# Performance work log

Measured on AMD Instinct MI355X. Metric: run time of the kernel, lower is better.

Reference implementation:

```python
import jax, jax.numpy as jnp
import numpy as np

E, K = 8, 2            # num_experts, top_k
H, DFF = 1024, 2048    # embd_dim, d_ff
B, S = 4, 1024


def setup_inputs() -> dict:
    key = jax.random.key(0)
    ks = jax.random.split(key, 5)
    s_in = 1.0 / np.sqrt(H)
    s_ff = 1.0 / np.sqrt(DFF)
    return {
        "x": jax.random.normal(ks[0], (B, S, H), jnp.float32),
        "centroids": jax.random.normal(ks[1], (E, H), jnp.float32),
        # nn.Linear weights are [out, in]
        "gate_w": jax.random.normal(ks[2], (E, DFF, H), jnp.float32) * s_in,
        "up_w": jax.random.normal(ks[3], (E, DFF, H), jnp.float32) * s_in,
        "down_w": jax.random.normal(ks[4], (E, H, DFF), jnp.float32) * s_ff,
        "routing_bias": jnp.zeros((E,), jnp.float32),
    }


def reference(x, centroids, gate_w, up_w, down_w, routing_bias):
    Bb, Ss, Hh = x.shape
    xf = x.reshape(-1, Hh)  # [T, H]
    # sigmoid affinity router + (non-trainable) routing bias
    affinity = jax.nn.sigmoid(xf @ centroids.T)          # [T, E]
    topk_scores, topk_idx = jax.lax.top_k(affinity + routing_bias, K)  # [T, K]
    topk_w = jax.nn.softmax(topk_scores, axis=-1)        # [T, K]

    # Dense per-expert SwiGLU FFN on all tokens (same math as the
    # sort/gather grouped loop; selection happens in the gather below).
    g = jnp.einsum('th,efh->etf', xf, gate_w)            # [E, T, DFF]
    u = jnp.einsum('th,efh->etf', xf, up_w)              # [E, T, DFF]
    y = jnp.einsum('etf,ehf->eth', jax.nn.silu(g) * u, down_w)  # [E, T, H]

    yt = jnp.transpose(y, (1, 0, 2))                     # [T, E, H]
    sel = jnp.take_along_axis(yt, topk_idx[:, :, None], axis=1)  # [T, K, H]
    out_flat = jnp.sum(sel * topk_w[:, :, None], axis=1)  # [T, H]

    counts = jnp.bincount(topk_idx.ravel(), length=E)    # per-expert token counts
    return out_flat.reshape(Bb, Ss, Hh), counts
```

## Files before the change

kernel.cpp:

```cpp
#include <hip/hip_runtime.h>
#include <math.h>

constexpr int E = 8, H = 1024, DFF = 2048, T = 4096;
constexpr int TR = 8192;
constexpr int MAXJ = 72;

typedef __bf16 bf16x8 __attribute__((ext_vector_type(8)));
typedef __bf16 bf16x4 __attribute__((ext_vector_type(4)));
typedef float f32x4 __attribute__((ext_vector_type(4)));

__device__ __forceinline__ void gload16(const void* g, void* l) {
    __builtin_amdgcn_global_load_lds(
        (const __attribute__((address_space(1))) unsigned int*)g,
        (__attribute__((address_space(3))) unsigned int*)l, 16, 0, 0);
}

constexpr int CONV_BLOCKS = 3072;
__global__ __launch_bounds__(256) void k0_fused(
    const float* __restrict__ x, const float* __restrict__ cent,
    const float* __restrict__ bias,
    int* __restrict__ se, float* __restrict__ sw,
    const float* __restrict__ gw, __bf16* __restrict__ gwb,
    const float* __restrict__ uw, __bf16* __restrict__ uwb,
    __bf16* __restrict__ xb, float* __restrict__ outz,
    int w4, int x4, int o4, int* __restrict__ done) {
    __shared__ float cs[E * H];
    int tid = threadIdx.x;

    if (blockIdx.x == 0 && tid == 0) *done = 0;

    if (blockIdx.x >= 1024) {
        int total = 2 * w4 + x4 + o4;
        int stride = CONV_BLOCKS * 256;
        for (int i = (blockIdx.x - 1024) * 256 + tid; i < total; i += stride) {
            if (i >= 2 * w4 + x4) {
                float4 z = {0.f, 0.f, 0.f, 0.f};
                ((float4*)outz)[i - 2 * w4 - x4] = z;
                continue;
            }
            const float* in; __bf16* outp; int idx;
            if (i < w4) { in = gw; outp = gwb; idx = i; }
            else if (i < 2 * w4) { in = uw; outp = uwb; idx = i - w4; }
            else { in = x; outp = xb; idx = i - 2 * w4; }
            float4 v = ((const float4*)in)[idx];
            bf16x4 o = {(__bf16)v.x, (__bf16)v.y, (__bf16)v.z, (__bf16)v.w};
            ((bf16x4*)outp)[idx] = o;
        }
        return;
    }

    for (int i = tid; i < E * H / 4; i += 256)
        ((float4*)cs)[i] = ((const float4*)cent)[i];
    __syncthreads();

    int wave = tid >> 6, lane = tid & 63;
    int t = blockIdx.x * 4 + wave;
    const float4* xr = (const float4*)(x + (size_t)t * H);
    float acc[E] = {};
    #pragma unroll
    for (int it = 0; it < 4; it++) {
        float4 xv = xr[lane + it * 64];
        #pragma unroll
        for (int e = 0; e < E; e++) {
            float4 cv = ((const float4*)(cs + e * H))[lane + it * 64];
            acc[e] = fmaf(xv.x, cv.x, acc[e]);
            acc[e] = fmaf(xv.y, cv.y, acc[e]);
            acc[e] = fmaf(xv.z, cv.z, acc[e]);
            acc[e] = fmaf(xv.w, cv.w, acc[e]);
        }
    }
    #pragma unroll
    for (int off = 32; off; off >>= 1)
        #pragma unroll
        for (int e = 0; e < E; e++) acc[e] += __shfl_down(acc[e], off);

    if (lane == 0) {
        float s[E];
        #pragma unroll
        for (int e = 0; e < E; e++)
            s[e] = 1.0f / (1.0f + expf(-acc[e])) + bias[e];
        int i0 = 0;
        for (int e = 1; e < E; e++) if (s[e] > s[i0]) i0 = e;
        int i1 = -1;
        for (int e = 0; e < E; e++) {
            if (e == i0) continue;
            if (i1 < 0 || s[e] > s[i1]) i1 = e;
        }
        float m = fmaxf(s[i0], s[i1]);
        float w0 = expf(s[i0] - m), w1 = expf(s[i1] - m);
        float inv = 1.0f / (w0 + w1);
        se[2 * t] = i0;     sw[2 * t] = w0 * inv;
        se[2 * t + 1] = i1; sw[2 * t + 1] = w1 * inv;
    }
}

__global__ __launch_bounds__(1024) void k1b_partition(
    const int* __restrict__ se, const float* __restrict__ sw,
    int* __restrict__ token_list, float* __restrict__ wlist,
    int* __restrict__ cnt,
    int* __restrict__ off, float* __restrict__ out_counts,
    int* __restrict__ jobs, int* __restrict__ njobs, int* __restrict__ done) {
    int e = blockIdx.x;
    int tid = threadIdx.x;
    int wave = tid >> 6, lane = tid & 63;
    __shared__ int wsum[16];
    int running = 0;
    for (int c0 = 0; c0 < 2 * T; c0 += 1024) {
        int i = c0 + tid;
        bool pred = (se[i] == e);
        unsigned long long mask = __ballot(pred);
        int pos_in_wave = __popcll(mask & ((1ull << lane) - 1ull));
        if (lane == 0) wsum[wave] = __popcll(mask);
        __syncthreads();
        int wbase = 0;
        #pragma unroll
        for (int w2 = 0; w2 < 16; w2++) {
            int v = wsum[w2];
            if (w2 < wave) wbase += v;
        }
        int total = 0;
        #pragma unroll
        for (int w2 = 0; w2 < 16; w2++) total += wsum[w2];
        if (pred) {
            int p = running + wbase + pos_in_wave;
            token_list[e * T + p] = i >> 1;
            wlist[e * T + p] = sw[i];
        }
        running += total;
        __syncthreads();
    }
    if (tid == 0) {
        __hip_atomic_store(&cnt[e], running, __ATOMIC_RELEASE, __HIP_MEMORY_SCOPE_AGENT);
        int prev = __hip_atomic_fetch_add(done, 1, __ATOMIC_ACQ_REL, __HIP_MEMORY_SCOPE_AGENT);
        if (prev == E - 1) {
            int acc = 0, nj = 0;
            for (int e2 = 0; e2 < E; e2++) {
                int c = __hip_atomic_load(&cnt[e2], __ATOMIC_ACQUIRE, __HIP_MEMORY_SCOPE_AGENT);
                off[e2] = acc; acc += c;
                out_counts[e2] = (float)c;
                int mts = (c + 127) >> 7;
                for (int mt = 0; mt < mts; mt++) jobs[nj++] = e2 * 64 + mt;
            }
            njobs[0] = nj;
        }
    }
}

constexpr int KCONV_BLOCKS = 1024;
__global__ __launch_bounds__(256) void k_conv(const float* __restrict__ in,
                                              __bf16* __restrict__ out, int n4) {
    int stride = KCONV_BLOCKS * 256;
    for (int i = blockIdx.x * 256 + threadIdx.x; i < n4; i += stride) {
        float4 v = ((const float4*)in)[i];
        bf16x4 o = {(__bf16)v.x, (__bf16)v.y, (__bf16)v.z, (__bf16)v.w};
        ((bf16x4*)out)[i] = o;
    }
}

__global__ __launch_bounds__(256, 2) void k2_gateup(
    const __bf16* __restrict__ xb, const __bf16* __restrict__ gwb,
    const __bf16* __restrict__ uwb, const int* __restrict__ cnt,
    const int* __restrict__ off, const int* __restrict__ token_list,
    const int* __restrict__ jobs, const int* __restrict__ njobs,
    __bf16* __restrict__ h) {
    int jt = blockIdx.x >> 4, nt = blockIdx.x & 15;
    if (jt >= njobs[0]) return;
    int job = jobs[jt];
    int e = job >> 6, mt = job & 63;
    int Me = cnt[e], offe = off[e];

    __shared__ __bf16 As[128 * 64];
    __shared__ __bf16 Bg[128 * 64];
    __shared__ __bf16 Bu[128 * 64];

    int tid = threadIdx.x;
    int lane = tid & 63, w = tid >> 6;
    int wm = w >> 1, wn = w & 1;

    const __bf16* asrc[4];
    const __bf16 *bsg[4], *bsu[4];
    #pragma unroll
    for (int rr = 0; rr < 4; rr++) {
        int l = rr * 256 + tid;
        int row = l >> 3, sl = l & 7;
        int gr = mt * 128 + row; if (gr >= Me) gr = Me - 1;
        int tok = token_list[e * T + gr];
        asrc[rr] = xb + (size_t)tok * H + ((sl ^ (row & 7)) * 8);
        size_t base = ((size_t)e * DFF + nt * 128 + row) * H + ((sl ^ (row & 7)) * 8);
        bsg[rr] = gwb + base;
        bsu[rr] = uwb + base;
    }

    f32x4 accg[4][4] = {};
    f32x4 accu[4][4] = {};
    int kq = lane >> 4, m15 = lane & 15;

    for (int k0 = 0; k0 < H; k0 += 64) {
        #pragma unroll
        for (int rr = 0; rr < 4; rr++) {
            gload16(asrc[rr] + k0, &As[(rr * 256 + tid) * 8]);
            gload16(bsg[rr] + k0, &Bg[(rr * 256 + tid) * 8]);
            gload16(bsu[rr] + k0, &Bu[(rr * 256 + tid) * 8]);
        }
        __syncthreads();

        #pragma unroll
        for (int kc = 0; kc < 2; kc++) {
            bf16x8 af[4], gf[4], uf[4];
            #pragma unroll
            for (int i = 0; i < 4; i++) {
                int row = wm * 64 + i * 16 + m15;
                int sl = (kc * 4 + kq) ^ (row & 7);
                af[i] = *(const bf16x8*)&As[row * 64 + sl * 8];
            }
            #pragma unroll
            for (int j = 0; j < 4; j++) {
                int row = wn * 64 + j * 16 + m15;
                int sl = (kc * 4 + kq) ^ (row & 7);
                gf[j] = *(const bf16x8*)&Bg[row * 64 + sl * 8];
                uf[j] = *(const bf16x8*)&Bu[row * 64 + sl * 8];
            }
            #pragma unroll
            for (int i = 0; i < 4; i++)
                #pragma unroll
                for (int j = 0; j < 4; j++) {
                    accg[i][j] = __builtin_amdgcn_mfma_f32_16x16x32_bf16(af[i], gf[j], accg[i][j], 0, 0, 0);
                    accu[i][j] = __builtin_amdgcn_mfma_f32_16x16x32_bf16(af[i], uf[j], accu[i][j], 0, 0, 0);
                }
        }
        __syncthreads();
    }

    #pragma unroll
    for (int i = 0; i < 4; i++)
        #pragma unroll
        for (int j = 0; j < 4; j++) {
            int nloc = wn * 64 + j * 16 + m15;
            size_t c = (size_t)nt * 128 + nloc;
            #pragma unroll
            for (int p = 0; p < 4; p++) {
                int mloc = wm * 64 + i * 16 + kq * 4 + p;
                int mrow = mt * 128 + mloc;
                if (mrow < Me) {
                    float g = accg[i][j][p], u = accu[i][j][p];
                    float sig = 1.0f / (1.0f + __expf(-g));
                    h[(size_t)(offe + mrow) * DFF + c] = (__bf16)(g * sig * u);
                }
            }
        }
}

__global__ __launch_bounds__(256, 2) void k3_down(
    const __bf16* __restrict__ h, const __bf16* __restrict__ dwb,
    const int* __restrict__ cnt, const int* __restrict__ off,
    const int* __restrict__ token_list, const float* __restrict__ wlist,
    const int* __restrict__ jobs, const int* __restrict__ njobs,
    float* __restrict__ out) {
    int jt = blockIdx.x >> 3, nt = blockIdx.x & 7;
    if (jt >= njobs[0]) return;
    int job = jobs[jt];
    int e = job >> 6, mt = job & 63;
    int Me = cnt[e], offe = off[e];

    __shared__ __bf16 As[128 * 64];
    __shared__ __bf16 Bs[128 * 64];

    int tid = threadIdx.x;
    int lane = tid & 63, w = tid >> 6;
    int wm = w >> 1, wn = w & 1;

    const __bf16* asrc[4];
    const __bf16* bsrc[4];
    #pragma unroll
    for (int rr = 0; rr < 4; rr++) {
        int l = rr * 256 + tid;
        int row = l >> 3, sl = l & 7;
        int koff = (sl ^ (row & 7)) * 8;
        int gr = mt * 128 + row; if (gr >= Me) gr = Me - 1;
        asrc[rr] = h + (size_t)(offe + gr) * DFF + koff;
        bsrc[rr] = dwb + ((size_t)e * H + nt * 128 + row) * DFF + koff;
    }

    f32x4 acc[4][4] = {};
    int kq = lane >> 4, m15 = lane & 15;

    for (int k0 = 0; k0 < DFF; k0 += 64) {
        #pragma unroll
        for (int rr = 0; rr < 4; rr++)
            gload16(asrc[rr] + k0, &As[(rr * 256 + tid) * 8]);
        #pragma unroll
        for (int rr = 0; rr < 4; rr++)
            gload16(bsrc[rr] + k0, &Bs[(rr * 256 + tid) * 8]);
        __syncthreads();

        #pragma unroll
        for (int kc = 0; kc < 2; kc++) {
            bf16x8 af[4], bf[4];
            #pragma unroll
            for (int i = 0; i < 4; i++) {
                int row = wm * 64 + i * 16 + m15;
                int sl = (kc * 4 + kq) ^ (row & 7);
                af[i] = *(const bf16x8*)&As[row * 64 + sl * 8];
            }
            #pragma unroll
            for (int j = 0; j < 4; j++) {
                int row = wn * 64 + j * 16 + m15;
                int sl = (kc * 4 + kq) ^ (row & 7);
                bf[j] = *(const bf16x8*)&Bs[row * 64 + sl * 8];
            }
            #pragma unroll
            for (int i = 0; i < 4; i++)
                #pragma unroll
                for (int j = 0; j < 4; j++)
                    acc[i][j] = __builtin_amdgcn_mfma_f32_16x16x32_bf16(af[i], bf[j], acc[i][j], 0, 0, 0);
        }
        __syncthreads();
    }

    #pragma unroll
    for (int i = 0; i < 4; i++) {
        #pragma unroll
        for (int p = 0; p < 4; p++) {
            int mloc = wm * 64 + i * 16 + kq * 4 + p;
            int mrow = mt * 128 + mloc;
            if (mrow < Me) {
                int tok = token_list[e * T + mrow];
                float wgt = wlist[e * T + mrow];
                float* orow = out + (size_t)tok * H;
                #pragma unroll
                for (int j = 0; j < 4; j++) {
                    int nglob = nt * 128 + wn * 64 + j * 16 + m15;
                    atomicAdd(&orow[nglob], wgt * acc[i][j][p]);
                }
            }
        }
    }
}

extern "C" void kernel_launch(void* const* d_in, const int* in_sizes, int n_in,
                              void* d_out, int out_size, void* d_ws, size_t ws_size,
                              hipStream_t stream) {
    const float* x    = (const float*)d_in[0];
    const float* cent = (const float*)d_in[1];
    const float* gw   = (const float*)d_in[2];
    const float* uw   = (const float*)d_in[3];
    const float* dw   = (const float*)d_in[4];
    const float* bias = (const float*)d_in[5];
    float* out = (float*)d_out;

    char* ws = (char*)d_ws;
    int*   cnt        = (int*)(ws + 0);
    int*   off        = (int*)(ws + 64);
    int*   se         = (int*)(ws + 128);
    float* sw         = (float*)(ws + 128 + 32768);
    int*   token_list = (int*)(ws + 128 + 65536);
    float* wlist      = (float*)(ws + 128 + 196608);
    int*   jobs       = (int*)(ws + 327808);
    int*   njobs      = (int*)(ws + 328128);
    int*   done       = (int*)(ws + 328192);
    const size_t MB = 1u << 20;
    __bf16* gwb = (__bf16*)(ws + 1 * MB);
    __bf16* uwb = (__bf16*)(ws + 1 * MB + 33554432);
    __bf16* dwb = gwb;
    __bf16* xb  = (__bf16*)(ws + 1 * MB + 67108864);
    __bf16* h   = (__bf16*)(ws + 1 * MB + 75497472);

    const int W4 = E * DFF * H / 4;
    const int X4 = T * H / 4;
    const int O4 = T * H / 4;

    k0_fused<<<1024 + CONV_BLOCKS, 256, 0, stream>>>(
        x, cent, bias, se, sw, gw, gwb, uw, uwb, xb, out, W4, X4, O4, done);
    k1b_partition<<<E, 1024, 0, stream>>>(se, sw, token_list, wlist, cnt,
                                          off, out + (size_t)T * H, jobs, njobs, done);
    k2_gateup<<<MAXJ * 16, 256, 0, stream>>>(xb, gwb, uwb, cnt, off, token_list, jobs, njobs, h);
    k_conv<<<KCONV_BLOCKS, 256, 0, stream>>>(dw, dwb, W4);
    k3_down<<<MAXJ * 8, 256, 0, stream>>>(h, dwb, cnt, off, token_list, wlist, jobs, njobs, out);
}
```

Before: 392.9 us.

## Fuse gate/up and down GEMMs into persistent ticketed kernel with per-job dependencies

Result: slower. 460.2 us (+17.1%).

```diff
diff --git a/kernel.cpp b/kernel.cpp
--- a/kernel.cpp
+++ b/kernel.cpp
@@ -4,6 +4,9 @@
 constexpr int E = 8, H = 1024, DFF = 2048, T = 4096;
 constexpr int TR = 8192;
 constexpr int MAXJ = 72;
+constexpr int NT2 = 16;
+constexpr int NT3 = 8;
+constexpr int PERS_BLOCKS = 768;
 
 typedef __bf16 bf16x8 __attribute__((ext_vector_type(8)));
 typedef __bf16 bf16x4 __attribute__((ext_vector_type(4)));
@@ -15,163 +18,16 @@
         (__attribute__((address_space(3))) unsigned int*)l, 16, 0, 0);
 }
 
-constexpr int CONV_BLOCKS = 3072;
-__global__ __launch_bounds__(256) void k0_fused(
-    const float* __restrict__ x, const float* __restrict__ cent,
-    const float* __restrict__ bias,
-    int* __restrict__ se, float* __restrict__ sw,
-    const float* __restrict__ gw, __bf16* __restrict__ gwb,
-    const float* __restrict__ uw, __bf16* __restrict__ uwb,
-    __bf16* __restrict__ xb, float* __restrict__ outz,
-    int w4, int x4, int o4, int* __restrict__ done) {
-    __shared__ float cs[E * H];
-    int tid = threadIdx.x;
-
-    if (blockIdx.x == 0 && tid == 0) *done = 0;
-
-    if (blockIdx.x >= 1024) {
-        int total = 2 * w4 + x4 + o4;
-        int stride = CONV_BLOCKS * 256;
-        for (int i = (blockIdx.x - 1024) * 256 + tid; i < total; i += stride) {
-            if (i >= 2 * w4 + x4) {
-                float4 z = {0.f, 0.f, 0.f, 0.f};
-                ((float4*)outz)[i - 2 * w4 - x4] = z;
-                continue;
-            }
-            const float* in; __bf16* outp; int idx;
-            if (i < w4) { in = gw; outp = gwb; idx = i; }
-            else if (i < 2 * w4) { in = uw; outp = uwb; idx = i - w4; }
-            else { in = x; outp = xb; idx = i - 2 * w4; }
-            float4 v = ((const float4*)in)[idx];
-            bf16x4 o = {(__bf16)v.x, (__bf16)v.y, (__bf16)v.z, (__bf16)v.w};
-            ((bf16x4*)outp)[idx] = o;
-        }
-        return;
-    }
-
-    for (int i = tid; i < E * H / 4; i += 256)
-        ((float4*)cs)[i] = ((const float4*)cent)[i];
-    __syncthreads();
-
-    int wave = tid >> 6, lane = tid & 63;
-    int t = blockIdx.x * 4 + wave;
-    const float4* xr = (const float4*)(x + (size_t)t * H);
-    float acc[E] = {};
-    #pragma unroll
-    for (int it = 0; it < 4; it++) {
-        float4 xv = xr[lane + it * 64];
-        #pragma unroll
-        for (int e = 0; e < E; e++) {
-            float4 cv = ((const float4*)(cs + e * H))[lane + it * 64];
-            acc[e] = fmaf(xv.x, cv.x, acc[e]);
-            acc[e] = fmaf(xv.y, cv.y, acc[e]);
-            acc[e] = fmaf(xv.z, cv.z, acc[e]);
-            acc[e] = fmaf(xv.w, cv.w, acc[e]);
-        }
-    }
-    #pragma unroll
-    for (int off = 32; off; off >>= 1)
-        #pragma unroll
-        for (int e = 0; e < E; e++) acc[e] += __shfl_down(acc[e], off);
-
-    if (lane == 0) {
-        float s[E];
-        #pragma unroll
-        for (int e = 0; e < E; e++)
-            s[e] = 1.0f / (1.0f + expf(-acc[e])) + bias[e];
-        int i0 = 0;
-        for (int e = 1; e < E; e++) if (s[e] > s[i0]) i0 = e;
-        int i1 = -1;
-        for (int e = 0; e < E; e++) {
-            if (e == i0) continue;
-            if (i1 < 0 || s[e] > s[i1]) i1 = e;
-        }
-        float m = fmaxf(s[i0], s[i1]);
-        float w0 = expf(s[i0] - m), w1 = expf(s[i1] - m);
-        float inv = 1.0f / (w0 + w1);
-        se[2 * t] = i0;     sw[2 * t] = w0 * inv;
-        se[2 * t + 1] = i1; sw[2 * t + 1] = w1 * inv;
-    }
-}
-
-__global__ __launch_bounds__(1024) void k1b_partition(
-    const int* __restrict__ se, const float* __restrict__ sw,
-    int* __restrict__ token_list, float* __restrict__ wlist,
-    int* __restrict__ cnt,
-    int* __restrict__ off, float* __restrict__ out_counts,
-    int* __restrict__ jobs, int* __restrict__ njobs, int* __restrict__ done) {
-    int e = blockIdx.x;
-    int tid = threadIdx.x;
-    int wave = tid >> 6, lane = tid & 63;
-    __shared__ int wsum[16];
-    int running = 0;
-    for (int c0 = 0; c0 < 2 * T; c0 += 1024) {
-        int i = c0 + tid;
-        bool pred = (se[i] == e);
-        unsigned long long mask = __ballot(pred);
-        int pos_in_wave = __popcll(mask & ((1ull << lane) - 1ull));
-        if (lane == 0) wsum[wave] = __popcll(mask);
-        __syncthreads();
-        int wbase = 0;
-        #pragma unroll
-        for (int w2 = 0; w2 < 16; w2++) {
-            int v = wsum[w2];
-            if (w2 < wave) wbase += v;
-        }
-        int total = 0;
-        #pragma unroll
-        for (int w2 = 0; w2 < 16; w2++) total += wsum[w2];
-        if (pred) {
-            int p = running + wbase + pos_in_wave;
-            token_list[e * T + p] = i >> 1;
-            wlist[e * T + p] = sw[i];
-        }
-        running += total;
-        __syncthreads();
-    }
-    if (tid == 0) {
-        __hip_atomic_store(&cnt[e], running, __ATOMIC_RELEASE, __HIP_MEMORY_SCOPE_AGENT);
-        int prev = __hip_atomic_fetch_add(done, 1, __ATOMIC_ACQ_REL, __HIP_MEMORY_SCOPE_AGENT);
-        if (prev == E - 1) {
-            int acc = 0, nj = 0;
-            for (int e2 = 0; e2 < E; e2++) {
-                int c = __hip_atomic_load(&cnt[e2], __ATOMIC_ACQUIRE, __HIP_MEMORY_SCOPE_AGENT);
-                off[e2] = acc; acc += c;
-                out_counts[e2] = (float)c;
-                int mts = (c + 127) >> 7;
-                for (int mt = 0; mt < mts; mt++) jobs[nj++] = e2 * 64 + mt;
-            }
-            njobs[0] = nj;
-        }
-    }
-}
-
-constexpr int KCONV_BLOCKS = 1024;
-__global__ __launch_bounds__(256) void k_conv(const float* __restrict__ in,
-                                              __bf16* __restrict__ out, int n4) {
-    int stride = KCONV_BLOCKS * 256;
-    for (int i = blockIdx.x * 256 + threadIdx.x; i < n4; i += stride) {
-        float4 v = ((const float4*)in)[i];
-        bf16x4 o = {(__bf16)v.x, (__bf16)v.y, (__bf16)v.z, (__bf16)v.w};
-        ((bf16x4*)out)[i] = o;
-    }
-}
-
-__global__ __launch_bounds__(256, 2) void k2_gateup(
+
+__device__ __forceinline__ void k2_task(
+    __bf16* As, __bf16* Bg, __bf16* Bu,
     const __bf16* __restrict__ xb, const __bf16* __restrict__ gwb,
     const __bf16* __restrict__ uwb, const int* __restrict__ cnt,
     const int* __restrict__ off, const int* __restrict__ token_list,
-    const int* __restrict__ jobs, const int* __restrict__ njobs,
-    __bf16* __restrict__ h) {
-    int jt = blockIdx.x >> 4, nt = blockIdx.x & 15;
-    if (jt >= njobs[0]) return;
+    const int* __restrict__ jobs, __bf16* __restrict__ h, int jt, int nt) {
     int job = jobs[jt];
     int e = job >> 6, mt = job & 63;
     int Me = cnt[e], offe = off[e];
-
-    __shared__ __bf16 As[128 * 64];
-    __shared__ __bf16 Bg[128 * 64];
-    __shared__ __bf16 Bu[128 * 64];
 
     int tid = threadIdx.x;
     int lane = tid & 63, w = tid >> 6;
@@ -250,20 +106,15 @@
         }
 }
 
-__global__ __launch_bounds__(256, 2) void k3_down(
+__device__ __forceinline__ void k3_task(
+    __bf16* As, __bf16* Bs,
     const __bf16* __restrict__ h, const __bf16* __restrict__ dwb,
     const int* __restrict__ cnt, const int* __restrict__ off,
     const int* __restrict__ token_list, const float* __restrict__ wlist,
-    const int* __restrict__ jobs, const int* __restrict__ njobs,
-    float* __restrict__ out) {
-    int jt = blockIdx.x >> 3, nt = blockIdx.x & 7;
-    if (jt >= njobs[0]) return;
+    const int* __restrict__ jobs, float* __restrict__ out, int jt, int nt) {
     int job = jobs[jt];
     int e = job >> 6, mt = job & 63;
     int Me = cnt[e], offe = off[e];
-
-    __shared__ __bf16 As[128 * 64];
-    __shared__ __bf16 Bs[128 * 64];
 
     int tid = threadIdx.x;
     int lane = tid & 63, w = tid >> 6;
@@ -337,6 +188,224 @@
     }
 }
 
+constexpr int CONV_BLOCKS = 3072;
+__global__ __launch_bounds__(256) void k0_fused(
+    const float* __restrict__ x, const float* __restrict__ cent,
+    const float* __restrict__ bias,
+    int* __restrict__ se, float* __restrict__ sw,
+    const float* __restrict__ gw, __bf16* __restrict__ gwb,
+    const float* __restrict__ uw, __bf16* __restrict__ uwb,
+    const float* __restrict__ dw, __bf16* __restrict__ dwb,
+    __bf16* __restrict__ xb, float* __restrict__ outz,
+    int w4, int x4, int o4, int* __restrict__ ctrl) {
+    __shared__ float cs[E * H];
+    int tid = threadIdx.x;
+
+    if (blockIdx.x == 0 && tid < 74) ctrl[tid] = 0;
+
+    if (blockIdx.x >= 1024) {
+        int nw = (dw != nullptr) ? 3 : 2;
+        int total = nw * w4 + x4 + o4;
+        int stride = CONV_BLOCKS * 256;
+        for (int i = (blockIdx.x - 1024) * 256 + tid; i < total; i += stride) {
+            if (i >= nw * w4 + x4) {
+                float4 z = {0.f, 0.f, 0.f, 0.f};
+                ((float4*)outz)[i - nw * w4 - x4] = z;
+                continue;
+            }
+            const float* in; __bf16* outp; int idx;
+            if (i < w4) { in = gw; outp = gwb; idx = i; }
+            else if (i < 2 * w4) { in = uw; outp = uwb; idx = i - w4; }
+            else if (nw == 3 && i < 3 * w4) { in = dw; outp = dwb; idx = i - 2 * w4; }
+            else { in = x; outp = xb; idx = i - nw * w4; }
+            float4 v = ((const float4*)in)[idx];
+            bf16x4 o = {(__bf16)v.x, (__bf16)v.y, (__bf16)v.z, (__bf16)v.w};
+            ((bf16x4*)outp)[idx] = o;
+        }
+        return;
+    }
+
+    for (int i = tid; i < E * H / 4; i += 256)
+        ((float4*)cs)[i] = ((const float4*)cent)[i];
+    __syncthreads();
+
+    int wave = tid >> 6, lane = tid & 63;
+    int t = blockIdx.x * 4 + wave;
+    const float4* xr = (const float4*)(x + (size_t)t * H);
+    float acc[E] = {};
+    #pragma unroll
+    for (int it = 0; it < 4; it++) {
+        float4 xv = xr[lane + it * 64];
+        #pragma unroll
+        for (int e = 0; e < E; e++) {
+            float4 cv = ((const float4*)(cs + e * H))[lane + it * 64];
+            acc[e] = fmaf(xv.x, cv.x, acc[e]);
+            acc[e] = fmaf(xv.y, cv.y, acc[e]);
+            acc[e] = fmaf(xv.z, cv.z, acc[e]);
+            acc[e] = fmaf(xv.w, cv.w, acc[e]);
+        }
+    }
+    #pragma unroll
+    for (int off = 32; off; off >>= 1)
+        #pragma unroll
+        for (int e = 0; e < E; e++) acc[e] += __shfl_down(acc[e], off);
+
+    if (lane == 0) {
+        float s[E];
+        #pragma unroll
+        for (int e = 0; e < E; e++)
+            s[e] = 1.0f / (1.0f + expf(-acc[e])) + bias[e];
+        int i0 = 0;
+        for (int e = 1; e < E; e++) if (s[e] > s[i0]) i0 = e;
+        int i1 = -1;
+        for (int e = 0; e < E; e++) {
+            if (e == i0) continue;
+            if (i1 < 0 || s[e] > s[i1]) i1 = e;
+        }
+        float m = fmaxf(s[i0], s[i1]);
+        float w0 = expf(s[i0] - m), w1 = expf(s[i1] - m);
+        float inv = 1.0f / (w0 + w1);
+        se[2 * t] = i0;     sw[2 * t] = w0 * inv;
+        se[2 * t + 1] = i1; sw[2 * t + 1] = w1 * inv;
+    }
+}
+
+__global__ __launch_bounds__(1024) void k1b_partition(
+    const int* __restrict__ se, const float* __restrict__ sw,
+    int* __restrict__ token_list, float* __restrict__ wlist,
+    int* __restrict__ cnt,
+    int* __restrict__ off, float* __restrict__ out_counts,
+    int* __restrict__ jobs, int* __restrict__ njobs, int* __restrict__ ctrl) {
+    int e = blockIdx.x;
+    int tid = threadIdx.x;
+    int wave = tid >> 6, lane = tid & 63;
+    __shared__ int wsum[16];
+    int running = 0;
+    for (int c0 = 0; c0 < 2 * T; c0 += 1024) {
+        int i = c0 + tid;
+        bool pred = (se[i] == e);
+        unsigned long long mask = __ballot(pred);
+        int pos_in_wave = __popcll(mask & ((1ull << lane) - 1ull));
+        if (lane == 0) wsum[wave] = __popcll(mask);
+        __syncthreads();
+        int wbase = 0;
+        #pragma unroll
+        for (int w2 = 0; w2 < 16; w2++) {
+            int v = wsum[w2];
+            if (w2 < wave) wbase += v;
+        }
+        int total = 0;
+        #pragma unroll
+        for (int w2 = 0; w2 < 16; w2++) total += wsum[w2];
+        if (pred) {
+            int p = running + wbase + pos_in_wave;
+            token_list[e * T + p] = i >> 1;
+            wlist[e * T + p] = sw[i];
+        }
+        running += total;
+        __syncthreads();
+    }
+    if (tid == 0) {
+        __hip_atomic_store(&cnt[e], running, __ATOMIC_RELEASE, __HIP_MEMORY_SCOPE_AGENT);
+        int prev = __hip_atomic_fetch_add(&ctrl[0], 1, __ATOMIC_ACQ_REL, __HIP_MEMORY_SCOPE_AGENT);
+        if (prev == E - 1) {
+            int acc = 0, nj = 0;
+            for (int e2 = 0; e2 < E; e2++) {
+                int c = __hip_atomic_load(&cnt[e2], __ATOMIC_ACQUIRE, __HIP_MEMORY_SCOPE_AGENT);
+                off[e2] = acc; acc += c;
+                out_counts[e2] = (float)c;
+                int mts = (c + 127) >> 7;
+                for (int mt = 0; mt < mts; mt++) jobs[nj++] = e2 * 64 + mt;
+            }
+            njobs[0] = nj;
+        }
+    }
+}
+
+constexpr int KCONV_BLOCKS = 1024;
+__global__ __launch_bounds__(256) void k_conv(const float* __restrict__ in,
+                                              __bf16* __restrict__ out, int n4) {
+    int stride = KCONV_BLOCKS * 256;
+    for (int i = blockIdx.x * 256 + threadIdx.x; i < n4; i += stride) {
+        float4 v = ((const float4*)in)[i];
+        bf16x4 o = {(__bf16)v.x, (__bf16)v.y, (__bf16)v.z, (__bf16)v.w};
+        ((bf16x4*)out)[i] = o;
+    }
+}
+
+__global__ __launch_bounds__(256, 2) void k23_fused(
+    const __bf16* __restrict__ xb, const __bf16* __restrict__ gwb,
+    const __bf16* __restrict__ uwb, const __bf16* __restrict__ dwb,
+    const int* __restrict__ cnt, const int* __restrict__ off,
+    const int* __restrict__ token_list, const float* __restrict__ wlist,
+    const int* __restrict__ jobs, const int* __restrict__ njobs,
+    __bf16* __restrict__ h, float* __restrict__ out, int* __restrict__ ctrl) {
+    __shared__ __bf16 As[128 * 64];
+    __shared__ __bf16 B0[128 * 64];
+    __shared__ __bf16 B1[128 * 64];
+    __shared__ int stick;
+
+    int tid = threadIdx.x;
+    int* ticket = &ctrl[1];
+    int* rg = &ctrl[2];
+
+    for (;;) {
+        __syncthreads();
+        if (tid == 0)
+            stick = __hip_atomic_fetch_add(ticket, 1, __ATOMIC_RELAXED, __HIP_MEMORY_SCOPE_AGENT);
+        __syncthreads();
+        int t = stick;
+        int nj = njobs[0];
+        int nk2 = nj * NT2, nk3 = nj * NT3;
+
+        if (t < nk2) {
+            int jt = t >> 4, nt = t & 15;
+            k2_task(As, B0, B1, xb, gwb, uwb, cnt, off, token_list, jobs, h, jt, nt);
+            __syncthreads();
+            if (tid == 0)
+                __hip_atomic_fetch_add(&rg[jt], 1, __ATOMIC_RELEASE, __HIP_MEMORY_SCOPE_AGENT);
+        } else if (t < nk2 + nk3) {
+            int t3 = t - nk2;
+            int jt = t3 >> 3, nt = t3 & 7;
+            if (tid == 0) {
+                while (__hip_atomic_load(&rg[jt], __ATOMIC_ACQUIRE, __HIP_MEMORY_SCOPE_AGENT) < NT2)
+                    __builtin_amdgcn_s_sleep(8);
+            }
+            __syncthreads();
+            k3_task(As, B0, h, dwb, cnt, off, token_list, wlist, jobs, out, jt, nt);
+        } else {
+            break;
+        }
+    }
+}
+
+__global__ __launch_bounds__(256, 2) void k2_gateup(
+    const __bf16* __restrict__ xb, const __bf16* __restrict__ gwb,
+    const __bf16* __restrict__ uwb, const int* __restrict__ cnt,
+    const int* __restrict__ off, const int* __restrict__ token_list,
+    const int* __restrict__ jobs, const int* __restrict__ njobs,
+    __bf16* __restrict__ h) {
+    int jt = blockIdx.x >> 4, nt = blockIdx.x & 15;
+    if (jt >= njobs[0]) return;
+    __shared__ __bf16 As[128 * 64];
+    __shared__ __bf16 Bg[128 * 64];
+    __shared__ __bf16 Bu[128 * 64];
+    k2_task(As, Bg, Bu, xb, gwb, uwb, cnt, off, token_list, jobs, h, jt, nt);
+}
+
+__global__ __launch_bounds__(256, 2) void k3_down(
+    const __bf16* __restrict__ h, const __bf16* __restrict__ dwb,
+    const int* __restrict__ cnt, const int* __restrict__ off,
+    const int* __restrict__ token_list, const float* __restrict__ wlist,
+    const int* __restrict__ jobs, const int* __restrict__ njobs,
+    float* __restrict__ out) {
+    int jt = blockIdx.x >> 3, nt = blockIdx.x & 7;
+    if (jt >= njobs[0]) return;
+    __shared__ __bf16 As[128 * 64];
+    __shared__ __bf16 Bs[128 * 64];
+    k3_task(As, Bs, h, dwb, cnt, off, token_list, wlist, jobs, out, jt, nt);
+}
+
 extern "C" void kernel_launch(void* const* d_in, const int* in_sizes, int n_in,
                               void* d_out, int out_size, void* d_ws, size_t ws_size,
                               hipStream_t stream) {
@@ -357,23 +426,41 @@
     float* wlist      = (float*)(ws + 128 + 196608);
     int*   jobs       = (int*)(ws + 327808);
     int*   njobs      = (int*)(ws + 328128);
-    int*   done       = (int*)(ws + 328192);
+    int*   ctrl       = (int*)(ws + 328192);
     const size_t MB = 1u << 20;
-    __bf16* gwb = (__bf16*)(ws + 1 * MB);
-    __bf16* uwb = (__bf16*)(ws + 1 * MB + 33554432);
-    __bf16* dwb = gwb;
-    __bf16* xb  = (__bf16*)(ws + 1 * MB + 67108864);
-    __bf16* h   = (__bf16*)(ws + 1 * MB + 75497472);
+
+    bool bigws = (ws_size >= 138 * MB);
+
+    __bf16 *gwb, *uwb, *dwb, *xb, *h;
+    if (bigws) {
+        gwb = (__bf16*)(ws + 1 * MB);
+        uwb = (__bf16*)(ws + 1 * MB + 33554432);
+        dwb = (__bf16*)(ws + 1 * MB + 67108864);
+        xb  = (__bf16*)(ws + 1 * MB + 100663296);
+        h   = (__bf16*)(ws + 1 * MB + 109051904);
+    } else {
+        gwb = (__bf16*)(ws + 1 * MB);
+        uwb = (__bf16*)(ws + 1 * MB + 33554432);
+        dwb = gwb;
+        xb  = (__bf16*)(ws + 1 * MB + 67108864);
+        h   = (__bf16*)(ws + 1 * MB + 75497472);
+    }
 
     const int W4 = E * DFF * H / 4;
     const int X4 = T * H / 4;
     const int O4 = T * H / 4;
 
     k0_fused<<<1024 + CONV_BLOCKS, 256, 0, stream>>>(
-        x, cent, bias, se, sw, gw, gwb, uw, uwb, xb, out, W4, X4, O4, done);
+        x, cent, bias, se, sw, gw, gwb, uw, uwb,
+        bigws ? dw : nullptr, dwb, xb, out, W4, X4, O4, ctrl);
     k1b_partition<<<E, 1024, 0, stream>>>(se, sw, token_list, wlist, cnt,
-                                          off, out + (size_t)T * H, jobs, njobs, done);
-    k2_gateup<<<MAXJ * 16, 256, 0, stream>>>(xb, gwb, uwb, cnt, off, token_list, jobs, njobs, h);
-    k_conv<<<KCONV_BLOCKS, 256, 0, stream>>>(dw, dwb, W4);
-    k3_down<<<MAXJ * 8, 256, 0, stream>>>(h, dwb, cnt, off, token_list, wlist, jobs, njobs, out);
-}
+                                          off, out + (size_t)T * H, jobs, njobs, ctrl);
+    if (bigws) {
+        k23_fused<<<PERS_BLOCKS, 256, 0, stream>>>(
+            xb, gwb, uwb, dwb, cnt, off, token_list, wlist, jobs, njobs, h, out, ctrl);
+    } else {
+        k2_gateup<<<MAXJ * 16, 256, 0, stream>>>(xb, gwb, uwb, cnt, off, token_list, jobs, njobs, h);
+        k_conv<<<KCONV_BLOCKS, 256, 0, stream>>>(dw, dwb, W4);
+        k3_down<<<MAXJ * 8, 256, 0, stream>>>(h, dwb, cnt, off, token_list, wlist, jobs, njobs, out);
+    }
+}
```
